# Kernel optimization log

Hardware: AMD Instinct MI355X
Metric: run time of the kernel (lower is better)

The kernel has to match this reference:

```python
import jax, jax.numpy as jnp
import numpy as np

DIMS = 256


def setup_inputs() -> dict:
    key = jax.random.key(0)
    ks = jax.random.split(key, 7)
    c = DIMS
    x = jax.random.normal(ks[0], (8, c, 64, 64), dtype=jnp.float32)
    s = 1.0 / np.sqrt(c)  # conv2d default init scale ~ U(-1/sqrt(fan_in),..)
    wq = jax.random.uniform(ks[1], (c, c), jnp.float32, -s, s)
    wk = jax.random.uniform(ks[2], (c, c), jnp.float32, -s, s)
    wv = jax.random.uniform(ks[3], (c, c), jnp.float32, -s, s)
    bq = jax.random.uniform(ks[4], (c,), jnp.float32, -s, s)
    bk = jax.random.uniform(ks[5], (c,), jnp.float32, -s, s)
    bv = jax.random.uniform(ks[6], (c,), jnp.float32, -s, s)
    return {"x": x, "wq": wq, "wk": wk, "wv": wv, "bq": bq, "bk": bk, "bv": bv}


def reference(x, wq, wk, wv, bq, bk, bv):
    b, c, h, w = x.shape
    xt = x.reshape(b, c, h * w).transpose(0, 2, 1)  # (b, hw, c)
    # 1x1 conv == per-pixel linear over channels; wq has shape (out_c, in_c)
    q = xt @ wq.T + bq  # (b, hw, c)
    k = xt @ wk.T + bk
    v = xt @ wv.T + bv
    scores = jnp.einsum('bnc,bmc->bnm', q, k) / jnp.sqrt(jnp.asarray(c, x.dtype))
    attn = jax.nn.softmax(scores, axis=-1)  # (b, hw, hw)
    out = jnp.einsum('bnm,bmc->bnc', attn, v)  # (b, hw, c)
    return out.transpose(0, 2, 1).reshape(b, c, h, w)
```

## Files before the change

kernel.cpp:

```cpp
#include <hip/hip_runtime.h>

#define NB 8
#define CC 256
#define NN 4096
#define KVB 64
#define NT (NN / KVB)

typedef __attribute__((ext_vector_type(8))) __bf16 bf16x8;
typedef __attribute__((ext_vector_type(4))) float f32x4;
typedef unsigned short u16;
typedef unsigned int u32;

#define GLL(g, l) __builtin_amdgcn_global_load_lds(                         \
    (const __attribute__((address_space(1))) void*)(g),                     \
    (__attribute__((address_space(3))) void*)(l), 16, 0, 0)

static __device__ __forceinline__ u16 f2b(float f) {
  unsigned u = __float_as_uint(f);
  u += 0x7FFF + ((u >> 16) & 1);
  return (u16)(u >> 16);
}

static __device__ __forceinline__ void plswap(u32& a, u32& b) {
  asm volatile("v_permlane32_swap_b32 %0, %1" : "+v"(a), "+v"(b));
}

__global__ __launch_bounds__(256) void k_prep(const float* __restrict__ x,
                                              u16* __restrict__ xb) {
  __shared__ float tile[64][65];
  const int b = blockIdx.z, c0 = blockIdx.y * 64, n0 = blockIdx.x * 64;
  const int t = threadIdx.x, j = t & 63, i0 = t >> 6;
  const float* xp = x + ((size_t)b * CC + c0) * NN + n0;
#pragma unroll
  for (int i = i0; i < 64; i += 4) tile[i][j] = xp[(size_t)i * NN + j];
  __syncthreads();
  u16* op = xb + ((size_t)b * NN + n0) * CC + c0;
#pragma unroll
  for (int r = i0; r < 64; r += 4) op[(size_t)r * CC + j] = f2b(tile[j][r]);
}

__global__ __launch_bounds__(256) void k_cvtw(const float* __restrict__ wq,
                                              const float* __restrict__ wk,
                                              const float* __restrict__ wv,
                                              u16* __restrict__ wb) {
  const int i = blockIdx.x * 256 + threadIdx.x;
  const int z = blockIdx.y;
  const float* s = z == 0 ? wq : (z == 1 ? wk : wv);
  wb[(size_t)z * CC * CC + i] = f2b(s[i]);
}

__global__ __launch_bounds__(256) void k_proj(const u16* __restrict__ xb,
                                              const u16* __restrict__ wb,
                                              const float* __restrict__ bq,
                                              const float* __restrict__ bk,
                                              const float* __restrict__ bv,
                                              u16* __restrict__ Qb,
                                              u16* __restrict__ Kb,
                                              u16* __restrict__ VTb) {
  const int z = blockIdx.z, b = blockIdx.y, n0 = blockIdx.x * 64;
  const u16* w = wb + (size_t)z * CC * CC;
  const float* bias = z == 0 ? bq : (z == 1 ? bk : bv);
  const float sc = z == 0 ? 0.09016844136959962f : 1.0f;
  const int wid = threadIdx.x >> 6, lane = threadIdx.x & 63;
  const int lr = lane & 15, lq = lane >> 4;
  const int i0 = wid * 64;
  const u16* A = xb + ((size_t)b * NN + n0) * CC;

  f32x4 acc[4][4];
#pragma unroll
  for (int mt = 0; mt < 4; ++mt)
#pragma unroll
    for (int it = 0; it < 4; ++it) acc[mt][it] = (f32x4){0.f, 0.f, 0.f, 0.f};

#pragma unroll
  for (int s = 0; s < 8; ++s) {
    const int kb = s * 32 + lq * 8;
    bf16x8 av[4], bm[4];
#pragma unroll
    for (int mt = 0; mt < 4; ++mt)
      av[mt] = *(const bf16x8*)(A + (size_t)(mt * 16 + lr) * CC + kb);
#pragma unroll
    for (int it = 0; it < 4; ++it)
      bm[it] = *(const bf16x8*)(w + (size_t)(i0 + it * 16 + lr) * CC + kb);
#pragma unroll
    for (int mt = 0; mt < 4; ++mt)
#pragma unroll
      for (int it = 0; it < 4; ++it)
        acc[mt][it] = __builtin_amdgcn_mfma_f32_16x16x32_bf16(av[mt], bm[it], acc[mt][it], 0, 0, 0);
  }

#pragma unroll
  for (int it = 0; it < 4; ++it) {
    const int i = i0 + it * 16 + lr;
    const float bb = bias[i];
#pragma unroll
    for (int mt = 0; mt < 4; ++mt) {
      f32x4 v = acc[mt][it];
      if (z == 2) {
        ushort4 p;
        p.x = f2b(v[0] + bb);
        p.y = f2b(v[1] + bb);
        p.z = f2b(v[2] + bb);
        p.w = f2b(v[3] + bb);
        *(ushort4*)(VTb + ((size_t)b * CC + i) * NN + n0 + mt * 16 + lq * 4) = p;
      } else {
        u16* O = (z == 0 ? Qb : Kb) + ((size_t)b * NN + n0 + mt * 16 + lq * 4) * CC + i;
#pragma unroll
        for (int r = 0; r < 4; ++r) O[(size_t)r * CC] = f2b((v[r] + bb) * sc);
      }
    }
  }
}

__global__ __launch_bounds__(512, 2) void k_attn(const u16* __restrict__ Qb,
                                                 const u16* __restrict__ Kb,
                                                 const u16* __restrict__ VTb,
                                                 float* __restrict__ out) {
  __shared__ __align__(16) u16 Kt[2][KVB * CC];
  __shared__ __align__(16) u16 Vt[2][CC * KVB];

  const int bid = blockIdx.x;
  const int b = bid & 7;
  const int q0 = (bid >> 3) * 128;
  const int tid = threadIdx.x;
  const int wid = tid >> 6, lane = tid & 63;
  const int lr = lane & 15, lq = lane >> 4;

  const char* Kbase = (const char*)(Kb + (size_t)b * NN * CC);
  const char* Vbase = (const char*)(VTb + (size_t)b * CC * NN);

  const int kc0 = wid * 4;
  const int krow_off = lane >> 5;
  const int kbyt = (lane & 31) * 16;
  const int vrow_off = lane >> 3;
  const int vbyt = (lane & 7) * 16;

  auto stage = [&](int buf, int kv) {
#pragma unroll
    for (int i = 0; i < 4; ++i) {
      const int c = kc0 + i;
      const int row = c * 2 + krow_off;
      GLL(Kbase + (size_t)(kv + row) * (CC * 2) + (kbyt ^ ((row & 7) << 4)),
          (char*)&Kt[buf][0] + c * 1024);
      const int vr = c * 8 + vrow_off;
      GLL(Vbase + (size_t)vr * (NN * 2) + (size_t)kv * 2 + (vbyt ^ ((vr & 7) << 4)),
          (char*)&Vt[buf][0] + c * 1024);
    }
  };

  stage(0, 0);

  bf16x8 qf[8];
  {
    const u16* Qp = Qb + ((size_t)b * NN + q0 + wid * 16 + lr) * CC + lq * 8;
#pragma unroll
    for (int s = 0; s < 8; ++s) qf[s] = *(const bf16x8*)(Qp + s * 32);
  }

  f32x4 oacc[16];
#pragma unroll
  for (int ct = 0; ct < 16; ++ct) oacc[ct] = (f32x4){0.f, 0.f, 0.f, 0.f};
  float lpart = 0.f;

  for (int t = 0; t < NT; ++t) {
    const int cur = t & 1;
    if (t + 1 < NT) {
      stage(cur ^ 1, (t + 1) * KVB);
      asm volatile("s_waitcnt vmcnt(8)" ::: "memory");
    } else {
      asm volatile("s_waitcnt vmcnt(0)" ::: "memory");
    }
    __builtin_amdgcn_s_barrier();

    f32x4 sacc[4];
#pragma unroll
    for (int jt = 0; jt < 4; ++jt) sacc[jt] = (f32x4){0.f, 0.f, 0.f, 0.f};
    __builtin_amdgcn_s_setprio(1);
#pragma unroll
    for (int s = 0; s < 8; ++s) {
      const int cb = s * 64 + lq * 16;
#pragma unroll
      for (int jt = 0; jt < 4; ++jt) {
        const int row = jt * 16 + lr;
        const bf16x8 kf = *(const bf16x8*)((const char*)&Kt[cur][0] +
                                           row * 512 + (cb ^ ((row & 7) << 4)));
        sacc[jt] = __builtin_amdgcn_mfma_f32_16x16x32_bf16(kf, qf[s], sacc[jt], 0, 0, 0);
      }
    }
    __builtin_amdgcn_s_setprio(0);

    u32 w[8];
#pragma unroll
    for (int jt = 0; jt < 4; ++jt) {
      const float p0 = __builtin_amdgcn_exp2f(sacc[jt][0]);
      const float p1 = __builtin_amdgcn_exp2f(sacc[jt][1]);
      const float p2 = __builtin_amdgcn_exp2f(sacc[jt][2]);
      const float p3 = __builtin_amdgcn_exp2f(sacc[jt][3]);
      lpart += (p0 + p1) + (p2 + p3);
      const __bf16 b0 = (__bf16)p0, b1 = (__bf16)p1, b2 = (__bf16)p2, b3 = (__bf16)p3;
      w[jt * 2]     = (u32)__builtin_bit_cast(u16, b0) | ((u32)__builtin_bit_cast(u16, b1) << 16);
      w[jt * 2 + 1] = (u32)__builtin_bit_cast(u16, b2) | ((u32)__builtin_bit_cast(u16, b3) << 16);
    }

    union { u32 u[4]; bf16x8 v; } pa0, pa1;
    const bool odd = (lq & 1);
#pragma unroll
    for (int ks = 0; ks < 2; ++ks) {
#pragma unroll
      for (int h = 0; h < 2; ++h) {
        u32 A = w[4 * ks + h], B = w[4 * ks + 2 + h];
        plswap(A, B);
        const u32 A16 = __builtin_amdgcn_ds_swizzle(A, 0x401F);
        const u32 B16 = __builtin_amdgcn_ds_swizzle(B, 0x401F);
        if (ks == 0) { pa0.u[h] = odd ? B16 : A; pa0.u[2 + h] = odd ? B : A16; }
        else         { pa1.u[h] = odd ? B16 : A; pa1.u[2 + h] = odd ? B : A16; }
      }
    }

    __builtin_amdgcn_s_setprio(1);
#pragma unroll
    for (int ks = 0; ks < 2; ++ks) {
      const bf16x8 pf = ks ? pa1.v : pa0.v;
#pragma unroll
      for (int ct = 0; ct < 16; ++ct) {
        const int row = ct * 16 + lr;
        const bf16x8 vf = *(const bf16x8*)((const char*)&Vt[cur][0] +
                                           row * 128 + ((ks * 64 + lq * 16) ^ ((row & 7) << 4)));
        oacc[ct] = __builtin_amdgcn_mfma_f32_16x16x32_bf16(pf, vf, oacc[ct], 0, 0, 0);
      }
    }
    __builtin_amdgcn_s_setprio(0);

    asm volatile("" ::: "memory");
    __builtin_amdgcn_s_barrier();
  }

  lpart += __shfl_xor(lpart, 16);
  lpart += __shfl_xor(lpart, 32);
  float linv[4];
#pragma unroll
  for (int r = 0; r < 4; ++r) linv[r] = 1.f / __shfl(lpart, lq * 20 + r);

  float* op = out + (size_t)b * CC * NN;
  const int nb = q0 + wid * 16 + lq * 4;
#pragma unroll
  for (int ct = 0; ct < 16; ++ct) {
    const int c = ct * 16 + lr;
    f32x4 v = {oacc[ct][0] * linv[0], oacc[ct][1] * linv[1],
               oacc[ct][2] * linv[2], oacc[ct][3] * linv[3]};
    *(f32x4*)(op + (size_t)c * NN + nb) = v;
  }
}

extern "C" void kernel_launch(void* const* d_in, const int* in_sizes, int n_in,
                              void* d_out, int out_size, void* d_ws, size_t ws_size,
                              hipStream_t stream) {
  const float* x = (const float*)d_in[0];
  const float* wq = (const float*)d_in[1];
  const float* wk = (const float*)d_in[2];
  const float* wv = (const float*)d_in[3];
  const float* bq = (const float*)d_in[4];
  const float* bk = (const float*)d_in[5];
  const float* bv = (const float*)d_in[6];
  float* out = (float*)d_out;

  u16* Qb = (u16*)d_ws;
  u16* Kb = Qb + (size_t)NB * NN * CC;
  u16* VTb = Kb + (size_t)NB * NN * CC;
  u16* wb = VTb + (size_t)NB * NN * CC;
  u16* xb = (u16*)d_out;

  k_prep<<<dim3(NN / 64, CC / 64, NB), 256, 0, stream>>>(x, xb);
  k_cvtw<<<dim3(CC * CC / 256, 3), 256, 0, stream>>>(wq, wk, wv, wb);
  k_proj<<<dim3(NN / 64, NB, 3), 256, 0, stream>>>(xb, wb, bq, bk, bv, Qb, Kb, VTb);
  k_attn<<<dim3(NN / 128 * NB), 512, 0, stream>>>(Qb, Kb, VTb, out);
}
```

Baseline: 245.0 us.

## Fuse transpose/convert into QKV projection and share x tile across Q,K,V

Removes the separate k_prep kernel that transposed x to a bf16 (n,c) buffer. The new k_qkv loads a 64-pixel fp32 slab of x directly, converts it to bf16 and stores it transposed into a swizzled LDS tile. It then computes all three projections from that tile in one block instead of three launches along z. This avoids writing and re-reading the intermediate xb buffer and re-reads x once rather than three times. The cost is fewer blocks (512 vs 1536) and a serialized z loop per block, which may reduce parallelism.

```diff
diff --git a/kernel.cpp b/kernel.cpp
--- a/kernel.cpp
+++ b/kernel.cpp
@@ -23,20 +23,6 @@
 
 static __device__ __forceinline__ void plswap(u32& a, u32& b) {
   asm volatile("v_permlane32_swap_b32 %0, %1" : "+v"(a), "+v"(b));
-}
-
-__global__ __launch_bounds__(256) void k_prep(const float* __restrict__ x,
-                                              u16* __restrict__ xb) {
-  __shared__ float tile[64][65];
-  const int b = blockIdx.z, c0 = blockIdx.y * 64, n0 = blockIdx.x * 64;
-  const int t = threadIdx.x, j = t & 63, i0 = t >> 6;
-  const float* xp = x + ((size_t)b * CC + c0) * NN + n0;
-#pragma unroll
-  for (int i = i0; i < 64; i += 4) tile[i][j] = xp[(size_t)i * NN + j];
-  __syncthreads();
-  u16* op = xb + ((size_t)b * NN + n0) * CC + c0;
-#pragma unroll
-  for (int r = i0; r < 64; r += 4) op[(size_t)r * CC + j] = f2b(tile[j][r]);
 }
 
 __global__ __launch_bounds__(256) void k_cvtw(const float* __restrict__ wq,
@@ -49,64 +35,87 @@
   wb[(size_t)z * CC * CC + i] = f2b(s[i]);
 }
 
-__global__ __launch_bounds__(256) void k_proj(const u16* __restrict__ xb,
-                                              const u16* __restrict__ wb,
-                                              const float* __restrict__ bq,
-                                              const float* __restrict__ bk,
-                                              const float* __restrict__ bv,
-                                              u16* __restrict__ Qb,
-                                              u16* __restrict__ Kb,
-                                              u16* __restrict__ VTb) {
-  const int z = blockIdx.z, b = blockIdx.y, n0 = blockIdx.x * 64;
-  const u16* w = wb + (size_t)z * CC * CC;
-  const float* bias = z == 0 ? bq : (z == 1 ? bk : bv);
-  const float sc = z == 0 ? 0.09016844136959962f : 1.0f;
-  const int wid = threadIdx.x >> 6, lane = threadIdx.x & 63;
+__global__ __launch_bounds__(256) void k_qkv(const float* __restrict__ x,
+                                             const u16* __restrict__ wb,
+                                             const float* __restrict__ bq,
+                                             const float* __restrict__ bk,
+                                             const float* __restrict__ bv,
+                                             u16* __restrict__ Qb,
+                                             u16* __restrict__ Kb,
+                                             u16* __restrict__ VTb) {
+  __shared__ __align__(16) u16 At[64 * 256];
+
+  const int b = blockIdx.y, n0 = blockIdx.x * 64;
+  const int tid = threadIdx.x;
+  const int wid = tid >> 6, lane = tid & 63;
   const int lr = lane & 15, lq = lane >> 4;
+
+  {
+    const int ccol = (lane & 15) * 4;
+#pragma unroll
+    for (int i = 0; i < 16; ++i) {
+      const int c = wid * 64 + i * 4 + (lane >> 4);
+      const f32x4 v = *(const f32x4*)(x + ((size_t)b * CC + c) * NN + n0 + ccol);
+#pragma unroll
+      for (int j = 0; j < 4; ++j) {
+        const int nr = ccol + j;
+        *(u16*)((char*)At + nr * 512 + ((c * 2) ^ ((nr & 7) << 4))) = f2b(v[j]);
+      }
+    }
+  }
+  __syncthreads();
+
   const int i0 = wid * 64;
-  const u16* A = xb + ((size_t)b * NN + n0) * CC;
-
-  f32x4 acc[4][4];
-#pragma unroll
-  for (int mt = 0; mt < 4; ++mt)
-#pragma unroll
-    for (int it = 0; it < 4; ++it) acc[mt][it] = (f32x4){0.f, 0.f, 0.f, 0.f};
-
-#pragma unroll
-  for (int s = 0; s < 8; ++s) {
-    const int kb = s * 32 + lq * 8;
-    bf16x8 av[4], bm[4];
+#pragma unroll
+  for (int z = 0; z < 3; ++z) {
+    const u16* w = wb + (size_t)z * CC * CC;
+    const float* bias = z == 0 ? bq : (z == 1 ? bk : bv);
+    const float sc = z == 0 ? 0.09016844136959962f : 1.0f;
+
+    f32x4 acc[4][4];
 #pragma unroll
     for (int mt = 0; mt < 4; ++mt)
-      av[mt] = *(const bf16x8*)(A + (size_t)(mt * 16 + lr) * CC + kb);
-#pragma unroll
-    for (int it = 0; it < 4; ++it)
-      bm[it] = *(const bf16x8*)(w + (size_t)(i0 + it * 16 + lr) * CC + kb);
-#pragma unroll
-    for (int mt = 0; mt < 4; ++mt)
+#pragma unroll
+      for (int it = 0; it < 4; ++it) acc[mt][it] = (f32x4){0.f, 0.f, 0.f, 0.f};
+
+#pragma unroll
+    for (int s = 0; s < 8; ++s) {
+      const int kb2 = s * 64 + lq * 16;
+      bf16x8 av[4], bm[4];
+#pragma unroll
+      for (int mt = 0; mt < 4; ++mt) {
+        const int row = mt * 16 + lr;
+        av[mt] = *(const bf16x8*)((const char*)At + row * 512 + (kb2 ^ ((row & 7) << 4)));
+      }
 #pragma unroll
       for (int it = 0; it < 4; ++it)
-        acc[mt][it] = __builtin_amdgcn_mfma_f32_16x16x32_bf16(av[mt], bm[it], acc[mt][it], 0, 0, 0);
-  }
-
-#pragma unroll
-  for (int it = 0; it < 4; ++it) {
-    const int i = i0 + it * 16 + lr;
-    const float bb = bias[i];
-#pragma unroll
-    for (int mt = 0; mt < 4; ++mt) {
-      f32x4 v = acc[mt][it];
-      if (z == 2) {
-        ushort4 p;
-        p.x = f2b(v[0] + bb);
-        p.y = f2b(v[1] + bb);
-        p.z = f2b(v[2] + bb);
-        p.w = f2b(v[3] + bb);
-        *(ushort4*)(VTb + ((size_t)b * CC + i) * NN + n0 + mt * 16 + lq * 4) = p;
-      } else {
-        u16* O = (z == 0 ? Qb : Kb) + ((size_t)b * NN + n0 + mt * 16 + lq * 4) * CC + i;
-#pragma unroll
-        for (int r = 0; r < 4; ++r) O[(size_t)r * CC] = f2b((v[r] + bb) * sc);
+        bm[it] = *(const bf16x8*)(w + (size_t)(i0 + it * 16 + lr) * CC + s * 32 + lq * 8);
+#pragma unroll
+      for (int mt = 0; mt < 4; ++mt)
+#pragma unroll
+        for (int it = 0; it < 4; ++it)
+          acc[mt][it] = __builtin_amdgcn_mfma_f32_16x16x32_bf16(av[mt], bm[it], acc[mt][it], 0, 0, 0);
+    }
+
+#pragma unroll
+    for (int it = 0; it < 4; ++it) {
+      const int i = i0 + it * 16 + lr;
+      const float bb = bias[i];
+#pragma unroll
+      for (int mt = 0; mt < 4; ++mt) {
+        f32x4 v = acc[mt][it];
+        if (z == 2) {
+          ushort4 p;
+          p.x = f2b(v[0] + bb);
+          p.y = f2b(v[1] + bb);
+          p.z = f2b(v[2] + bb);
+          p.w = f2b(v[3] + bb);
+          *(ushort4*)(VTb + ((size_t)b * CC + i) * NN + n0 + mt * 16 + lq * 4) = p;
+        } else {
+          u16* O = (z == 0 ? Qb : Kb) + ((size_t)b * NN + n0 + mt * 16 + lq * 4) * CC + i;
+#pragma unroll
+          for (int r = 0; r < 4; ++r) O[(size_t)r * CC] = f2b((v[r] + bb) * sc);
+        }
       }
     }
   }
@@ -268,10 +277,8 @@
   u16* Kb = Qb + (size_t)NB * NN * CC;
   u16* VTb = Kb + (size_t)NB * NN * CC;
   u16* wb = VTb + (size_t)NB * NN * CC;
-  u16* xb = (u16*)d_out;
-
-  k_prep<<<dim3(NN / 64, CC / 64, NB), 256, 0, stream>>>(x, xb);
+
   k_cvtw<<<dim3(CC * CC / 256, 3), 256, 0, stream>>>(wq, wk, wv, wb);
-  k_proj<<<dim3(NN / 64, NB, 3), 256, 0, stream>>>(xb, wb, bq, bk, bv, Qb, Kb, VTb);
+  k_qkv<<<dim3(NN / 64, NB), 256, 0, stream>>>(x, wb, bq, bk, bv, Qb, Kb, VTb);
   k_attn<<<dim3(NN / 128 * NB), 512, 0, stream>>>(Qb, Kb, VTb, out);
 }
```

Measured after the change: 223.1 us. 1.1x faster.
